# Optimization experiments

Measured on AMD Instinct MI355X. Metric: run time of the kernel, lower is better.

The kernel has to match this reference:

```python
import jax, jax.numpy as jnp
import numpy as np


def setup_inputs() -> dict:
    key = jax.random.key(0)
    k1, k2, k3 = jax.random.split(key, 3)
    N = 50000
    E = 1600000
    D = 128
    indices = jax.random.randint(k1, (2, E), 0, N, dtype=jnp.int64)
    values = jax.random.uniform(k2, (E,), dtype=jnp.float32)
    b = jax.random.normal(k3, (N, D), dtype=jnp.float32)
    return {"indices": indices, "values": values, "n": N, "b": b}


def reference(indices, values, n, b):
    # out = A @ b where A is sparse COO: A[row[e], col[e]] = values[e]
    rows = indices[0]  # [E]
    cols = indices[1]  # [E]
    # gather source features per edge, scale by edge value, scatter-add to rows
    contrib = values[:, None] * b[cols]  # [E, D]
    out = jax.ops.segment_sum(contrib, rows, num_segments=n)  # [N, D]
    return out
```

## Files before the change

### kernel.cpp

```cpp
#include <hip/hip_runtime.h>
#include <hip/hip_bf16.h>


#define D_DIM  128
#define CSLOT  48
#define SPILL_CAP (1 << 18)

__global__ __launch_bounds__(256) void cvt_kernel(const float* __restrict__ b,
                                                  ushort* __restrict__ b16, int n8) {
    int i = blockIdx.x * 256 + threadIdx.x;
    int stride = gridDim.x * 256;
    for (; i < n8; i += stride) {
        float4 f0 = *reinterpret_cast<const float4*>(b + (size_t)i * 8);
        float4 f1 = *reinterpret_cast<const float4*>(b + (size_t)i * 8 + 4);
        uint u[8] = {__float_as_uint(f0.x), __float_as_uint(f0.y),
                     __float_as_uint(f0.z), __float_as_uint(f0.w),
                     __float_as_uint(f1.x), __float_as_uint(f1.y),
                     __float_as_uint(f1.z), __float_as_uint(f1.w)};
        uint r[8];
        #pragma unroll
        for (int k = 0; k < 8; ++k)
            r[k] = (u[k] + 0x7fffu + ((u[k] >> 16) & 1u)) >> 16;
        uint4 w;
        w.x = r[0] | (r[1] << 16);
        w.y = r[2] | (r[3] << 16);
        w.z = r[4] | (r[5] << 16);
        w.w = r[6] | (r[7] << 16);
        *reinterpret_cast<uint4*>(b16 + (size_t)i * 8) = w;
    }
}

__global__ __launch_bounds__(256) void scatter_slots(const int* __restrict__ rows,
                                                     const int* __restrict__ cols,
                                                     const float* __restrict__ vals,
                                                     int* __restrict__ rowcnt,
                                                     int* __restrict__ spill_cnt,
                                                     int2* __restrict__ spill,
                                                     int2* __restrict__ slots, int E) {
    int chunk = blockIdx.x >> 3;
    int slice = blockIdx.x & 7;
    int e = chunk * 256 + threadIdx.x;
    if (e >= E) return;
    int r = rows[e];
    if (((r >> 5) & 7) != slice) return;
    int c = cols[e];
    int v = __float_as_int(vals[e]);
    int pos = atomicAdd(&rowcnt[r], 1);
    if (pos < CSLOT) {
        slots[r * CSLOT + pos] = make_int2(c, v);
    } else {
        int sp = atomicAdd(spill_cnt, 1);
        if (sp < SPILL_CAP)
            spill[sp] = make_int2((r << 16) | c, v);
    }
}

__device__ inline void bf16_fma4(float4& acc, float v, uint2 u) {
    float f0 = __uint_as_float(u.x << 16);
    float f1 = __uint_as_float(u.x & 0xffff0000u);
    float f2 = __uint_as_float(u.y << 16);
    float f3 = __uint_as_float(u.y & 0xffff0000u);
    acc.x = fmaf(v, f0, acc.x);
    acc.y = fmaf(v, f1, acc.y);
    acc.z = fmaf(v, f2, acc.z);
    acc.w = fmaf(v, f3, acc.w);
}

__global__ __launch_bounds__(256) void reduce_slots_b16(const int* __restrict__ rowcnt,
                                                        const int2* __restrict__ slots,
                                                        const ushort* __restrict__ b16,
                                                        float* __restrict__ out, int n) {
    const int x    = blockIdx.x & 7;
    const int rest = blockIdx.x >> 3;
    const int jq   = rest & 7;
    const int k    = rest >> 3;
    const int g    = k * 8 + x;
    const int row  = g * 32 + jq * 4 + (threadIdx.x >> 6);
    if (row >= n) return;

    const int lane = threadIdx.x & 63;
    const int half = lane >> 5;
    const int l32  = lane & 31;

    int cnt = __builtin_amdgcn_readfirstlane(rowcnt[row]);
    if (cnt > CSLOT) cnt = CSLOT;
    const int s = row * CSLOT;
    const int e = s + cnt;

    const ushort* bl = b16 + l32 * 4;
    float4 acc = make_float4(0.f, 0.f, 0.f, 0.f);

    int j = s;
    for (; j + 16 <= e; j += 16) {
        int cc[8]; float vv[8];
        #pragma unroll
        for (int k2 = 0; k2 < 8; ++k2) {
            int2 a0 = slots[j + 2 * k2];
            int2 a1 = slots[j + 2 * k2 + 1];
            cc[k2] = half ? a1.x : a0.x;
            vv[k2] = __int_as_float(half ? a1.y : a0.y);
        }
        uint2 bv[8];
        #pragma unroll
        for (int k2 = 0; k2 < 8; ++k2)
            bv[k2] = *reinterpret_cast<const uint2*>(bl + (size_t)cc[k2] * D_DIM);
        #pragma unroll
        for (int k2 = 0; k2 < 8; ++k2) bf16_fma4(acc, vv[k2], bv[k2]);
    }
    for (; j + 4 <= e; j += 4) {
        int2 a0 = slots[j],     a1 = slots[j + 1];
        int2 a2 = slots[j + 2], a3 = slots[j + 3];
        int   c0 = half ? a1.x : a0.x;
        float v0 = __int_as_float(half ? a1.y : a0.y);
        int   c1 = half ? a3.x : a2.x;
        float v1 = __int_as_float(half ? a3.y : a2.y);
        uint2 u0 = *reinterpret_cast<const uint2*>(bl + (size_t)c0 * D_DIM);
        uint2 u1 = *reinterpret_cast<const uint2*>(bl + (size_t)c1 * D_DIM);
        bf16_fma4(acc, v0, u0);
        bf16_fma4(acc, v1, u1);
    }
    for (; j + 2 <= e; j += 2) {
        int2 a0 = slots[j], a1 = slots[j + 1];
        int   c = half ? a1.x : a0.x;
        float v = __int_as_float(half ? a1.y : a0.y);
        uint2 u = *reinterpret_cast<const uint2*>(bl + (size_t)c * D_DIM);
        bf16_fma4(acc, v, u);
    }
    if (j < e) {
        int2 a0 = slots[j];
        int   c = half ? 0 : a0.x;
        float v = half ? 0.f : __int_as_float(a0.y);
        uint2 u = *reinterpret_cast<const uint2*>(bl + (size_t)c * D_DIM);
        bf16_fma4(acc, v, u);
    }
    acc.x += __shfl_xor(acc.x, 32, 64);
    acc.y += __shfl_xor(acc.y, 32, 64);
    acc.z += __shfl_xor(acc.z, 32, 64);
    acc.w += __shfl_xor(acc.w, 32, 64);
    if (half == 0)
        *reinterpret_cast<float4*>(out + (size_t)row * D_DIM + l32 * 4) = acc;
}

__global__ __launch_bounds__(256) void spill_apply(const int2* __restrict__ spill,
                                                   const int* __restrict__ spill_cnt,
                                                   const float* __restrict__ b,
                                                   float* __restrict__ out) {
    int total = *spill_cnt;
    if (total > SPILL_CAP) total = SPILL_CAP;
    const int lane  = threadIdx.x & 63;
    const int wid   = (blockIdx.x * 256 + threadIdx.x) >> 6;
    const int nwave = (gridDim.x * 256) >> 6;
    for (int i = wid; i < total; i += nwave) {
        int2 a = spill[i];
        int r = (int)((unsigned)a.x >> 16);
        int c = a.x & 0xffff;
        float v = __int_as_float(a.y);
        float2 bb = *reinterpret_cast<const float2*>(b + (size_t)c * D_DIM + lane * 2);
        atomicAdd(&out[(size_t)r * D_DIM + lane * 2],     v * bb.x);
        atomicAdd(&out[(size_t)r * D_DIM + lane * 2 + 1], v * bb.y);
    }
}

__global__ __launch_bounds__(256) void zero_kernel(float* __restrict__ out, size_t n4) {
    size_t i = (size_t)blockIdx.x * 256 + threadIdx.x;
    size_t stride = (size_t)gridDim.x * 256;
    for (; i < n4; i += stride)
        reinterpret_cast<float4*>(out)[i] = make_float4(0.f, 0.f, 0.f, 0.f);
}

__global__ __launch_bounds__(256) void atomic_spmm_kernel(const int* __restrict__ rows,
                                                          const int* __restrict__ cols,
                                                          const float* __restrict__ vals,
                                                          const float* __restrict__ b,
                                                          float* __restrict__ out, int E) {
    long long t = (long long)blockIdx.x * 256 + threadIdx.x;
    int e = (int)(t >> 5);
    int q = (int)(t & 31);
    if (e >= E) return;
    int   r = rows[e];
    int   c = cols[e];
    float v = vals[e];
    float4 bb = *reinterpret_cast<const float4*>(b + (size_t)c * D_DIM + q * 4);
    float* o = out + (size_t)r * D_DIM + q * 4;
    atomicAdd(o + 0, v * bb.x);
    atomicAdd(o + 1, v * bb.y);
    atomicAdd(o + 2, v * bb.z);
    atomicAdd(o + 3, v * bb.w);
}

extern "C" void kernel_launch(void* const* d_in, const int* in_sizes, int n_in,
                              void* d_out, int out_size, void* d_ws, size_t ws_size,
                              hipStream_t stream) {
    const int*   idx  = (const int*)d_in[0];
    const float* vals = (const float*)d_in[1];
    const float* b    = (const float*)d_in[3];
    float*       out  = (float*)d_out;

    const int E = in_sizes[1];
    const int N = in_sizes[3] / D_DIM;
    const int* rows = idx;
    const int* cols = idx + E;

    size_t spill_off = (((size_t)(N + 1) * sizeof(int)) + 15) & ~(size_t)15;
    size_t slots_off = spill_off + (size_t)SPILL_CAP * sizeof(int2);
    size_t b16_off   = slots_off + (size_t)N * CSLOT * sizeof(int2);
    size_t need      = b16_off + (size_t)N * D_DIM * sizeof(ushort);

    if (ws_size >= need && N <= 65536) {
        char*   ws        = (char*)d_ws;
        int*    rowcnt    = (int*)ws;
        int*    spill_cnt = rowcnt + N;
        int2*   spill     = (int2*)(ws + spill_off);
        int2*   slots     = (int2*)(ws + slots_off);
        ushort* b16       = (ushort*)(ws + b16_off);

        hipMemsetAsync(rowcnt, 0, (size_t)(N + 1) * sizeof(int), stream);
        cvt_kernel<<<2048, 256, 0, stream>>>(b, b16, N * D_DIM / 8);
        int eb = (E + 255) / 256;
        scatter_slots<<<eb * 8, 256, 0, stream>>>(rows, cols, vals, rowcnt,
                                                  spill_cnt, spill, slots, E);
        int kmax  = ((N + 31) / 32 + 7) / 8;
        int rgrid = 8 * 8 * kmax;
        reduce_slots_b16<<<rgrid, 256, 0, stream>>>(rowcnt, slots, b16, out, N);
        spill_apply<<<64, 256, 0, stream>>>(spill, spill_cnt, b, out);
    } else {
        size_t n4 = (size_t)N * D_DIM / 4;
        zero_kernel<<<2048, 256, 0, stream>>>(out, n4);
        long long total = (long long)E * 32;
        int ab = (int)((total + 255) / 256);
        atomic_spmm_kernel<<<ab, 256, 0, stream>>>(rows, cols, vals, b, out, E);
    }
}
```

Measured before the change: 235.0 us.

## Split slot buckets per XCD, pack col with bf16 value, merge in LDS

The scatter pass no longer launches eight redundant block copies that each read every edge and filter by row slice. Each block now reads four edges per thread with vector loads and appends them to one of eight per-XCD slot arrays, chosen by block index. Each slot entry is packed into 32 bits: a 16-bit column and a bf16 value. The reduce kernel gathers the eight sub-buckets of a row into shared memory before the bf16 gather-FMA loop. This cuts edge-read traffic, slot storage and contention on the atomic counters, at the cost of rounding edge values to bf16 and an 8x larger counter memset.

```diff
diff --git a/kernel.cpp b/kernel.cpp
--- a/kernel.cpp
+++ b/kernel.cpp
@@ -2,9 +2,14 @@
 #include <hip/hip_bf16.h>
 
 
-#define D_DIM  128
-#define CSLOT  48
-#define SPILL_CAP (1 << 18)
+#define D_DIM 128
+#define CSX   16
+#define SPILL_CAP (1 << 16)
+
+__device__ inline uint f32_to_bf16(float f) {
+    uint u = __float_as_uint(f);
+    return (u + 0x7fffu + ((u >> 16) & 1u)) >> 16;
+}
 
 __global__ __launch_bounds__(256) void cvt_kernel(const float* __restrict__ b,
                                                   ushort* __restrict__ b16, int n8) {
@@ -13,14 +18,10 @@
     for (; i < n8; i += stride) {
         float4 f0 = *reinterpret_cast<const float4*>(b + (size_t)i * 8);
         float4 f1 = *reinterpret_cast<const float4*>(b + (size_t)i * 8 + 4);
-        uint u[8] = {__float_as_uint(f0.x), __float_as_uint(f0.y),
-                     __float_as_uint(f0.z), __float_as_uint(f0.w),
-                     __float_as_uint(f1.x), __float_as_uint(f1.y),
-                     __float_as_uint(f1.z), __float_as_uint(f1.w)};
-        uint r[8];
-        #pragma unroll
-        for (int k = 0; k < 8; ++k)
-            r[k] = (u[k] + 0x7fffu + ((u[k] >> 16) & 1u)) >> 16;
+        uint r[8] = {f32_to_bf16(f0.x), f32_to_bf16(f0.y),
+                     f32_to_bf16(f0.z), f32_to_bf16(f0.w),
+                     f32_to_bf16(f1.x), f32_to_bf16(f1.y),
+                     f32_to_bf16(f1.z), f32_to_bf16(f1.w)};
         uint4 w;
         w.x = r[0] | (r[1] << 16);
         w.y = r[2] | (r[3] << 16);
@@ -30,28 +31,54 @@
     }
 }
 
-__global__ __launch_bounds__(256) void scatter_slots(const int* __restrict__ rows,
-                                                     const int* __restrict__ cols,
-                                                     const float* __restrict__ vals,
-                                                     int* __restrict__ rowcnt,
-                                                     int* __restrict__ spill_cnt,
-                                                     int2* __restrict__ spill,
-                                                     int2* __restrict__ slots, int E) {
-    int chunk = blockIdx.x >> 3;
-    int slice = blockIdx.x & 7;
-    int e = chunk * 256 + threadIdx.x;
-    if (e >= E) return;
-    int r = rows[e];
-    if (((r >> 5) & 7) != slice) return;
-    int c = cols[e];
-    int v = __float_as_int(vals[e]);
-    int pos = atomicAdd(&rowcnt[r], 1);
-    if (pos < CSLOT) {
-        slots[r * CSLOT + pos] = make_int2(c, v);
+__global__ __launch_bounds__(256) void scatter_x(const int* __restrict__ rows,
+                                                 const int* __restrict__ cols,
+                                                 const float* __restrict__ vals,
+                                                 int* __restrict__ rowcnt,
+                                                 int* __restrict__ spill_cnt,
+                                                 int2* __restrict__ spill,
+                                                 uint* __restrict__ slots,
+                                                 int E, int N) {
+    const int  t = threadIdx.x;
+    const int  x = blockIdx.x & 7;
+    int*  cntx  = rowcnt + (size_t)x * N;
+    uint* slotx = slots + (size_t)x * N * CSX;
+    long e0 = (long)blockIdx.x * 1024 + t * 4;
+    if (e0 + 3 < E) {
+        int4   r4 = *reinterpret_cast<const int4*>(rows + e0);
+        int4   c4 = *reinterpret_cast<const int4*>(cols + e0);
+        float4 v4 = *reinterpret_cast<const float4*>(vals + e0);
+        int   rr[4] = {r4.x, r4.y, r4.z, r4.w};
+        int   cc[4] = {c4.x, c4.y, c4.z, c4.w};
+        float vv[4] = {v4.x, v4.y, v4.z, v4.w};
+        #pragma unroll
+        for (int k = 0; k < 4; ++k) {
+            int pos = atomicAdd(&cntx[rr[k]], 1);
+            uint w  = ((uint)cc[k] << 16) | f32_to_bf16(vv[k]);
+            if (pos < CSX) {
+                slotx[(size_t)rr[k] * CSX + pos] = w;
+            } else {
+                int sp = atomicAdd(spill_cnt, 1);
+                if (sp < SPILL_CAP)
+                    spill[sp] = make_int2((rr[k] << 16) | cc[k], __float_as_int(vv[k]));
+            }
+        }
     } else {
-        int sp = atomicAdd(spill_cnt, 1);
-        if (sp < SPILL_CAP)
-            spill[sp] = make_int2((r << 16) | c, v);
+        for (int k = 0; k < 4; ++k) {
+            long e = e0 + k;
+            if (e >= E) break;
+            int r = rows[e], c = cols[e];
+            float v = vals[e];
+            int pos = atomicAdd(&cntx[r], 1);
+            uint w  = ((uint)c << 16) | f32_to_bf16(v);
+            if (pos < CSX) {
+                slotx[(size_t)r * CSX + pos] = w;
+            } else {
+                int sp = atomicAdd(spill_cnt, 1);
+                if (sp < SPILL_CAP)
+                    spill[sp] = make_int2((r << 16) | c, __float_as_int(v));
+            }
+        }
     }
 }
 
@@ -66,72 +93,62 @@
     acc.w = fmaf(v, f3, acc.w);
 }
 
-__global__ __launch_bounds__(256) void reduce_slots_b16(const int* __restrict__ rowcnt,
-                                                        const int2* __restrict__ slots,
-                                                        const ushort* __restrict__ b16,
-                                                        float* __restrict__ out, int n) {
-    const int x    = blockIdx.x & 7;
-    const int rest = blockIdx.x >> 3;
-    const int jq   = rest & 7;
-    const int k    = rest >> 3;
-    const int g    = k * 8 + x;
-    const int row  = g * 32 + jq * 4 + (threadIdx.x >> 6);
-    if (row >= n) return;
-
+__global__ __launch_bounds__(256) void reduce_x(const int* __restrict__ rowcnt,
+                                                const uint* __restrict__ slots,
+                                                const ushort* __restrict__ b16,
+                                                float* __restrict__ out, int N) {
+    __shared__ uint sbuf[4][8 * CSX];
+    const int w    = threadIdx.x >> 6;
     const int lane = threadIdx.x & 63;
     const int half = lane >> 5;
     const int l32  = lane & 31;
-
-    int cnt = __builtin_amdgcn_readfirstlane(rowcnt[row]);
-    if (cnt > CSLOT) cnt = CSLOT;
-    const int s = row * CSLOT;
-    const int e = s + cnt;
+    const int row  = blockIdx.x * 4 + w;
+    if (row >= N) return;
+
+    int tot = 0;
+    #pragma unroll
+    for (int x = 0; x < 8; ++x) {
+        int cx = __builtin_amdgcn_readfirstlane(rowcnt[(size_t)x * N + row]);
+        if (cx > CSX) cx = CSX;
+        if (lane < cx)
+            sbuf[w][tot + lane] = slots[((size_t)x * N + row) * CSX + lane];
+        tot += cx;
+    }
 
     const ushort* bl = b16 + l32 * 4;
     float4 acc = make_float4(0.f, 0.f, 0.f, 0.f);
-
-    int j = s;
-    for (; j + 16 <= e; j += 16) {
-        int cc[8]; float vv[8];
-        #pragma unroll
-        for (int k2 = 0; k2 < 8; ++k2) {
-            int2 a0 = slots[j + 2 * k2];
-            int2 a1 = slots[j + 2 * k2 + 1];
-            cc[k2] = half ? a1.x : a0.x;
-            vv[k2] = __int_as_float(half ? a1.y : a0.y);
-        }
+    int j = 0;
+    for (; j + 16 <= tot; j += 16) {
+        uint uu[8];
+        #pragma unroll
+        for (int k = 0; k < 8; ++k) uu[k] = sbuf[w][j + 2 * k + half];
         uint2 bv[8];
         #pragma unroll
-        for (int k2 = 0; k2 < 8; ++k2)
-            bv[k2] = *reinterpret_cast<const uint2*>(bl + (size_t)cc[k2] * D_DIM);
-        #pragma unroll
-        for (int k2 = 0; k2 < 8; ++k2) bf16_fma4(acc, vv[k2], bv[k2]);
-    }
-    for (; j + 4 <= e; j += 4) {
-        int2 a0 = slots[j],     a1 = slots[j + 1];
-        int2 a2 = slots[j + 2], a3 = slots[j + 3];
-        int   c0 = half ? a1.x : a0.x;
-        float v0 = __int_as_float(half ? a1.y : a0.y);
-        int   c1 = half ? a3.x : a2.x;
-        float v1 = __int_as_float(half ? a3.y : a2.y);
-        uint2 u0 = *reinterpret_cast<const uint2*>(bl + (size_t)c0 * D_DIM);
-        uint2 u1 = *reinterpret_cast<const uint2*>(bl + (size_t)c1 * D_DIM);
-        bf16_fma4(acc, v0, u0);
-        bf16_fma4(acc, v1, u1);
-    }
-    for (; j + 2 <= e; j += 2) {
-        int2 a0 = slots[j], a1 = slots[j + 1];
-        int   c = half ? a1.x : a0.x;
-        float v = __int_as_float(half ? a1.y : a0.y);
-        uint2 u = *reinterpret_cast<const uint2*>(bl + (size_t)c * D_DIM);
-        bf16_fma4(acc, v, u);
-    }
-    if (j < e) {
-        int2 a0 = slots[j];
-        int   c = half ? 0 : a0.x;
-        float v = half ? 0.f : __int_as_float(a0.y);
-        uint2 u = *reinterpret_cast<const uint2*>(bl + (size_t)c * D_DIM);
-        bf16_fma4(acc, v, u);
+        for (int k = 0; k < 8; ++k)
+            bv[k] = *reinterpret_cast<const uint2*>(bl + (size_t)(uu[k] >> 16) * D_DIM);
+        #pragma unroll
+        for (int k = 0; k < 8; ++k)
+            bf16_fma4(acc, __uint_as_float(uu[k] << 16), bv[k]);
+    }
+    for (; j + 4 <= tot; j += 4) {
+        uint u0 = sbuf[w][j + half];
+        uint u1 = sbuf[w][j + 2 + half];
+        uint2 b0 = *reinterpret_cast<const uint2*>(bl + (size_t)(u0 >> 16) * D_DIM);
+        uint2 b1 = *reinterpret_cast<const uint2*>(bl + (size_t)(u1 >> 16) * D_DIM);
+        bf16_fma4(acc, __uint_as_float(u0 << 16), b0);
+        bf16_fma4(acc, __uint_as_float(u1 << 16), b1);
+    }
+    for (; j + 2 <= tot; j += 2) {
+        uint u = sbuf[w][j + half];
+        uint2 bb = *reinterpret_cast<const uint2*>(bl + (size_t)(u >> 16) * D_DIM);
+        bf16_fma4(acc, __uint_as_float(u << 16), bb);
+    }
+    if (j < tot) {
+        uint u = sbuf[w][j];
+        uint  c = half ? 0u : (u >> 16);
+        float v = half ? 0.f : __uint_as_float(u << 16);
+        uint2 bb = *reinterpret_cast<const uint2*>(bl + (size_t)c * D_DIM);
+        bf16_fma4(acc, v, bb);
     }
     acc.x += __shfl_xor(acc.x, 32, 64);
     acc.y += __shfl_xor(acc.y, 32, 64);
@@ -201,27 +218,25 @@
     const int* rows = idx;
     const int* cols = idx + E;
 
-    size_t spill_off = (((size_t)(N + 1) * sizeof(int)) + 15) & ~(size_t)15;
+    size_t spill_off = (((size_t)(8 * (size_t)N + 1) * sizeof(int)) + 15) & ~(size_t)15;
     size_t slots_off = spill_off + (size_t)SPILL_CAP * sizeof(int2);
-    size_t b16_off   = slots_off + (size_t)N * CSLOT * sizeof(int2);
+    size_t b16_off   = slots_off + 8 * (size_t)N * CSX * sizeof(uint);
     size_t need      = b16_off + (size_t)N * D_DIM * sizeof(ushort);
 
     if (ws_size >= need && N <= 65536) {
         char*   ws        = (char*)d_ws;
         int*    rowcnt    = (int*)ws;
-        int*    spill_cnt = rowcnt + N;
+        int*    spill_cnt = rowcnt + 8 * (size_t)N;
         int2*   spill     = (int2*)(ws + spill_off);
-        int2*   slots     = (int2*)(ws + slots_off);
+        uint*   slots     = (uint*)(ws + slots_off);
         ushort* b16       = (ushort*)(ws + b16_off);
 
-        hipMemsetAsync(rowcnt, 0, (size_t)(N + 1) * sizeof(int), stream);
+        hipMemsetAsync(rowcnt, 0, (8 * (size_t)N + 1) * sizeof(int), stream);
         cvt_kernel<<<2048, 256, 0, stream>>>(b, b16, N * D_DIM / 8);
-        int eb = (E + 255) / 256;
-        scatter_slots<<<eb * 8, 256, 0, stream>>>(rows, cols, vals, rowcnt,
-                                                  spill_cnt, spill, slots, E);
-        int kmax  = ((N + 31) / 32 + 7) / 8;
-        int rgrid = 8 * 8 * kmax;
-        reduce_slots_b16<<<rgrid, 256, 0, stream>>>(rowcnt, slots, b16, out, N);
+        int sb = (int)((E + 1023) / 1024);
+        scatter_x<<<sb, 256, 0, stream>>>(rows, cols, vals, rowcnt,
+                                          spill_cnt, spill, slots, E, N);
+        reduce_x<<<(N + 3) / 4, 256, 0, stream>>>(rowcnt, slots, b16, out, N);
         spill_apply<<<64, 256, 0, stream>>>(spill, spill_cnt, b, out);
     } else {
         size_t n4 = (size_t)N * D_DIM / 4;
```

Measured after the change: 273.2 us. +16.3%, slower.
